# Kernel tuning notes

Hardware: AMD Instinct MI355X
Metric: run time of the kernel (lower is better)

## Reference

```python
import jax, jax.numpy as jnp
import numpy as np

B, L, D = 4, 2048, 64
N_HEAD = 4
LOCALITY = 0.2
PI = 3.141592653589793


def setup_inputs() -> dict:
    key = jax.random.key(0)
    k1, k2, k3 = jax.random.split(key, 3)
    mesh = jax.random.uniform(k1, (B, L, 2), dtype=jnp.float32)
    inputs = jax.random.normal(k2, (B, L, D), dtype=jnp.float32)
    lmda = jax.random.uniform(k3, (N_HEAD, 1, 1), dtype=jnp.float32)
    return {"mesh": mesh, "inputs": inputs, "lmda": lmda}


def reference(mesh, inputs, lmda):
    FMAX = jnp.finfo(jnp.float32).max
    # pairwise squared distances: (B, L, L)
    diff = mesh[:, :, None, :] - mesh[:, None, :, :]
    m_dist = jnp.sum(diff * diff, axis=-1)
    # per-head scale in (0, inf): tan(pi/4 * (1-eps) * (1 + sin(lmda)))
    scale = jnp.tan(0.25 * PI * (1.0 - 1e-07) * (1.0 + jnp.sin(lmda)))  # (H,1,1)
    scaled = m_dist[:, None, :, :] * scale  # (B, H, L, L)
    # row-wise quantile threshold (linear interpolation, matching torch.quantile)
    thresh = jnp.quantile(scaled, LOCALITY, axis=-1, keepdims=True)  # (B,H,L,1)
    masked = jnp.where(scaled <= thresh, scaled, FMAX)
    att = jax.nn.softmax(-masked, axis=-1)  # (B, H, L, L)
    # aggregate: (B,H,L,L) x (B,L,D) -> (B,L,H,D) -> (B,L,H*D)
    conv = jnp.einsum('bhnj,bjd->bnhd', att, inputs)
    conv = conv.reshape(inputs.shape[0], -1, N_HEAD * inputs.shape[-1])
    return jnp.concatenate([inputs, conv], axis=-1)
```

## Files before the change

kernel.cpp:

```cpp
#include <hip/hip_runtime.h>
#include <math.h>

#ifndef M_PI
#define M_PI 3.14159265358979323846
#endif

namespace {
constexpr int B_ = 4;
constexpr int L_ = 2048;
constexpr int D_ = 64;
constexpr int H_ = 4;
constexpr int RB = 8;
constexpr int KT = 64;
constexpr int NTILE = L_ / KT;
constexpr int CAPC = 256;
constexpr int OUTW = D_ + H_ * D_;
constexpr int APS = 2064;
}

typedef __attribute__((ext_vector_type(8))) short bf16x8;
typedef __attribute__((ext_vector_type(4))) float f32x4;

__device__ __forceinline__ unsigned bf16_rne(float x) {
    unsigned u = __float_as_uint(x);
    return (u + 0x7fffu + ((u >> 16) & 1u)) >> 16;
}

#define LDS_FENCE() __builtin_amdgcn_s_waitcnt(0xC07F)

__global__ __launch_bounds__(512, 8) void posatt_kernel(
    const float* __restrict__ mesh,
    const float* __restrict__ inputs,
    const float* __restrict__ lmda,
    float* __restrict__ out)
{
    __shared__ __align__(16) float2 s_mesh[L_];
    __shared__ __align__(16) char s_u1[16448];
    __shared__ float s_scale[H_];
    __shared__ float s_th[RB][H_];
    __shared__ float s_d409[RB], s_d410[RB];
    __shared__ float s_wsum[RB][H_];
    __shared__ unsigned s_ccw[8];

    const int t = threadIdx.x;
    const int l = t & 63;
    const int w = t >> 6;
    const int blk = blockIdx.x;
    const int b = blk >> 8;
    const int n0 = (blk & 255) * RB;

    if (t < H_) {
        const double lam = (double)lmda[t];
        const float C = (float)(0.25 * M_PI * (1.0 - 1e-07));
        const float s1 = (float)sin(lam);
        const float arg = __fmul_rn(C, __fadd_rn(1.0f, s1));
        s_scale[t] = (float)tan((double)arg);
    }
    {
        const float4* mg = reinterpret_cast<const float4*>(mesh + (size_t)b * L_ * 2);
        float4* msd = reinterpret_cast<float4*>(s_mesh);
        msd[t] = mg[t];
        msd[t + 512] = mg[t + 512];
    }
    __syncthreads();

    {
        unsigned* hw = reinterpret_cast<unsigned*>(s_u1) + w * 256;
        float* cw = reinterpret_cast<float*>(s_u1 + 8192) + w * CAPC;
        const int rl = w;
        const float2 me = s_mesh[n0 + rl];
        *reinterpret_cast<uint4*>(&hw[l * 4]) = make_uint4(0u, 0u, 0u, 0u);
        if (l == 0) s_ccw[w] = 0u;
        LDS_FENCE();
        #pragma unroll 1
        for (int it = 0; it < 32; ++it) {
            const int j = (it << 6) + l;
            const float2 mj = s_mesh[j];
            const float dx = __fsub_rn(me.x, mj.x);
            const float dy = __fsub_rn(me.y, mj.y);
            const float d = __fadd_rn(__fmul_rn(dx, dx), __fmul_rn(dy, dy));
            int bin = (int)(d * 128.0f); bin = bin < 255 ? bin : 255;
            atomicAdd(&hw[bin], 1u);
        }
        LDS_FENCE();
        const uint4 hv = *reinterpret_cast<const uint4*>(&hw[l * 4]);
        const unsigned p0 = hv.x, p1 = p0 + hv.y, p2 = p1 + hv.z, p3 = p2 + hv.w;
        unsigned sc = p3;
        #pragma unroll
        for (int off = 1; off < 64; off <<= 1) {
            const unsigned uu = __shfl_up(sc, off);
            if (l >= off) sc += uu;
        }
        const unsigned eb = sc - p3;
        const unsigned cum[4] = {eb + p0, eb + p1, eb + p2, eb + p3};
        int flo = -1, fhi = -1; unsigned fbase = 0u;
        #pragma unroll
        for (int e = 0; e < 4; ++e) {
            const unsigned prev = e ? cum[e - 1] : eb;
            if (cum[e] > 409u && prev <= 409u) { flo = l * 4 + e; fbase = prev; }
            if (cum[e] > 410u && prev <= 410u) { fhi = l * 4 + e; }
        }
        const unsigned long long bmlo = __ballot(flo >= 0);
        const int srclo = (int)__builtin_ctzll(bmlo);
        const int lo = __shfl(flo, srclo);
        const unsigned base = __shfl(fbase, srclo);
        const unsigned long long bmhi = __ballot(fhi >= 0);
        const int hi = __shfl(fhi, (int)__builtin_ctzll(bmhi));
        #pragma unroll 1
        for (int it = 0; it < 32; ++it) {
            const int j = (it << 6) + l;
            const float2 mj = s_mesh[j];
            const float dx = __fsub_rn(me.x, mj.x);
            const float dy = __fsub_rn(me.y, mj.y);
            const float d = __fadd_rn(__fmul_rn(dx, dx), __fmul_rn(dy, dy));
            int bin = (int)(d * 128.0f); bin = bin < 255 ? bin : 255;
            if (bin >= lo && bin <= hi) {
                const unsigned p = atomicAdd(&s_ccw[w], 1u);
                if (p < (unsigned)CAPC) cw[p] = d;
            }
        }
        LDS_FENCE();
        const int m = (int)min(s_ccw[w], (unsigned)CAPC);
        const int k409 = 409 - (int)base;
        const int k410 = 410 - (int)base;
        #pragma unroll 1
        for (int cc0 = 0; cc0 < m; cc0 += 64) {
            const int ci = cc0 + l;
            const float v = (ci < m) ? cw[ci] : 0.0f;
            int lt = 0, le = 0;
            #pragma unroll 1
            for (int i = 0; i < m; ++i) {
                const float u = cw[i];
                lt += (u < v) ? 1 : 0;
                le += (u <= v) ? 1 : 0;
            }
            if (ci < m) {
                if (lt <= k409 && k409 < le) s_d409[rl] = v;
                if (lt <= k410 && k410 < le) s_d410[rl] = v;
            }
        }
    }
    __syncthreads();

    if (t < RB * H_) {
        const int r = t >> 2, h = t & 3;
        const float scl = s_scale[h];
        const float s409 = __fmul_rn(s_d409[r], scl);
        const float s410 = __fmul_rn(s_d410[r], scl);
        const float pos = 0.2f * 2047.0f;
        const float g = pos - 409.0f;
        const float lw = 1.0f - g;
        s_th[r][h] = __fadd_rn(__fmul_rn(s409, lw), __fmul_rn(s410, g));
    }
    __syncthreads();

    const int mr   = t >> 4;
    const int h_b  = mr >> 3;
    const int r_b  = mr & 7;
    const int jg   = t & 15;
    const int row16 = ((h_b & 1) << 3) + r_b;
    const int pln   = h_b >> 1;
    const float2 me_b = s_mesh[n0 + r_b];
    const float sc_b = s_scale[h_b];
    const float th_b = s_th[r_b][h_b];
    const int aoff = pln * APS + ((((jg >> 3) * 4 + ((jg >> 1) & 3)) * 16 + row16) << 4) + ((jg & 1) << 3);
    float wacc = 0.0f;

    const int p_w  = w >> 2;
    const int ks_w = (w >> 1) & 1;
    const int nqh  = w & 1;
    f32x4 acc[2];
    acc[0] = (f32x4)0.0f; acc[1] = (f32x4)0.0f;

    const float* inpb = inputs + (size_t)b * L_ * D_;
    char* Abase = s_u1;
    char* Bbase = s_u1 + 2 * APS;

    #pragma unroll 1
    for (int tile = 0; tile < NTILE; ++tile) {
        __syncthreads();
        unsigned pk0[4];
        {
            const int kb0 = tile * KT + ((t >> 6) << 3);
            const float* pb0 = inpb + (size_t)kb0 * D_ + (t & 63);
            #pragma unroll
            for (int e2 = 0; e2 < 4; ++e2) {
                const float xa = pb0[(2 * e2) * D_];
                const float xb = pb0[(2 * e2 + 1) * D_];
                pk0[e2] = bf16_rne(xa) | (bf16_rne(xb) << 16);
            }
        }
        const int k0 = tile * KT;
        {
            const float4 mq0 = *reinterpret_cast<const float4*>(&s_mesh[k0 + jg * 4]);
            const float4 mq1 = *reinterpret_cast<const float4*>(&s_mesh[k0 + jg * 4 + 2]);
            const float dx0 = __fsub_rn(me_b.x, mq0.x);
            const float dy0 = __fsub_rn(me_b.y, mq0.y);
            const float d0 = __fadd_rn(__fmul_rn(dx0, dx0), __fmul_rn(dy0, dy0));
            const float dx1 = __fsub_rn(me_b.x, mq0.z);
            const float dy1 = __fsub_rn(me_b.y, mq0.w);
            const float d1 = __fadd_rn(__fmul_rn(dx1, dx1), __fmul_rn(dy1, dy1));
            const float dx2 = __fsub_rn(me_b.x, mq1.x);
            const float dy2 = __fsub_rn(me_b.y, mq1.y);
            const float d2 = __fadd_rn(__fmul_rn(dx2, dx2), __fmul_rn(dy2, dy2));
            const float dx3 = __fsub_rn(me_b.x, mq1.z);
            const float dy3 = __fsub_rn(me_b.y, mq1.w);
            const float d3 = __fadd_rn(__fmul_rn(dx3, dx3), __fmul_rn(dy3, dy3));
            const float x0 = __fmul_rn(d0, sc_b);
            const float x1 = __fmul_rn(d1, sc_b);
            const float x2 = __fmul_rn(d2, sc_b);
            const float x3 = __fmul_rn(d3, sc_b);
            const float w0 = (x0 <= th_b) ? __expf(-x0) : 0.0f;
            const float w1 = (x1 <= th_b) ? __expf(-x1) : 0.0f;
            const float w2 = (x2 <= th_b) ? __expf(-x2) : 0.0f;
            const float w3 = (x3 <= th_b) ? __expf(-x3) : 0.0f;
            wacc += (w0 + w1) + (w2 + w3);
            const unsigned u01 = bf16_rne(w0) | (bf16_rne(w1) << 16);
            const unsigned u23 = bf16_rne(w2) | (bf16_rne(w3) << 16);
            *reinterpret_cast<uint2*>(Abase + aoff) = make_uint2(u01, u23);
        }
        *reinterpret_cast<uint4*>(Bbase + t * 16) = make_uint4(pk0[0], pk0[1], pk0[2], pk0[3]);
        __syncthreads();
        const bf16x8 afr = *reinterpret_cast<const bf16x8*>(
            Abase + p_w * APS + (((ks_w * 4 + (l >> 4)) * 16 + (l & 15)) << 4));
        #pragma unroll
        for (int i = 0; i < 2; ++i) {
            const int nq = nqh * 2 + i;
            const bf16x8 bfr = *reinterpret_cast<const bf16x8*>(
                Bbase + (((ks_w * 4 + (l >> 4)) * 64 + nq * 16 + (l & 15)) << 4));
            acc[i] = __builtin_amdgcn_mfma_f32_16x16x32_bf16(afr, bfr, acc[i], 0, 0, 0);
        }
    }
    __syncthreads();

    wacc += __shfl_xor(wacc, 1);
    wacc += __shfl_xor(wacc, 2);
    wacc += __shfl_xor(wacc, 4);
    wacc += __shfl_xor(wacc, 8);
    if ((l & 15) == 0) s_wsum[r_b][h_b] = wacc;
    {
        float4* Cz = reinterpret_cast<float4*>(s_u1);
        Cz[t] = make_float4(0.f, 0.f, 0.f, 0.f);
    }
    __syncthreads();
    {
        float* Cf = reinterpret_cast<float*>(s_u1);
        #pragma unroll
        for (int i = 0; i < 2; ++i) {
            const int nq = nqh * 2 + i;
            #pragma unroll
            for (int reg = 0; reg < 4; ++reg) {
                const int row = (l >> 4) * 4 + reg;
                const int col = nq * 16 + (l & 15);
                atomicAdd(&Cf[(p_w * 16 + row) * 64 + col], acc[i][reg]);
            }
        }
    }
    __syncthreads();
    {
        const float* Cf = reinterpret_cast<const float*>(s_u1);
        const int pr = t >> 4;
        const int p = pr >> 4;
        const int row16o = pr & 15;
        const int h = p * 2 + (row16o >> 3);
        const int r = row16o & 7;
        const int col = (t & 15) << 2;
        const float wsv = s_wsum[r][h];
        const float inv = (wsv != 0.0f) ? 1.0f / wsv : 0.0f;
        float4 r0 = *reinterpret_cast<const float4*>(&Cf[pr * 64 + col]);
        r0.x *= inv; r0.y *= inv; r0.z *= inv; r0.w *= inv;
        float* op = out + (size_t)(b * L_ + n0 + r) * OUTW + D_ + h * 64 + col;
        *reinterpret_cast<float4*>(op) = r0;
    }
    {
        const int r = t >> 6;
        const int c = t & 63;
        out[(size_t)(b * L_ + n0 + r) * OUTW + c] = inpb[(size_t)(n0 + r) * D_ + c];
    }
}

extern "C" void kernel_launch(void* const* d_in, const int* in_sizes, int n_in,
                              void* d_out, int out_size, void* d_ws, size_t ws_size,
                              hipStream_t stream) {
    const float* mesh   = (const float*)d_in[0];
    const float* inputs = (const float*)d_in[1];
    const float* lmda   = (const float*)d_in[2];
    float* out = (float*)d_out;
    (void)in_sizes; (void)n_in; (void)out_size; (void)d_ws; (void)ws_size;
    hipLaunchKernelGGL(posatt_kernel, dim3(B_ * (L_ / RB)), dim3(512), 0, stream,
                       mesh, inputs, lmda, out);
}
```

Measured before the change: 146.5 us.

## Pre-convert inputs to bf16 tiled layout in a prep kernel; XOR-swizzle A tile in LDS

```diff
diff --git a/kernel.cpp b/kernel.cpp
--- a/kernel.cpp
+++ b/kernel.cpp
@@ -28,10 +28,37 @@
 
 #define LDS_FENCE() __builtin_amdgcn_s_waitcnt(0xC07F)
 
+__global__ __launch_bounds__(256) void prep_kernel(const float* __restrict__ inputs,
+                                                   char* __restrict__ ws) {
+    const int blk = blockIdx.x;
+    const int b = blk >> 6;
+    const int r6 = blk & 63;
+    const int tile = r6 >> 2;
+    const int qr = r6 & 3;
+    const int t = threadIdx.x;
+    const float* inb = inputs + ((size_t)b * L_ + tile * 128) * D_;
+    char* wsb = ws + (size_t)b * (L_ * D_ * 2) + tile * (128 * D_ * 2);
+    #pragma unroll
+    for (int i = 0; i < 4; ++i) {
+        const int idx = qr * 1024 + i * 256 + t;
+        const int n  = idx & 63;
+        const int kp = idx >> 6;
+        const int kl = kp << 1;
+        const float x0 = inb[kl * D_ + n];
+        const float x1 = inb[(kl + 1) * D_ + n];
+        const unsigned a = bf16_rne(x0);
+        const unsigned c = bf16_rne(x1);
+        const int chunk = (kl >> 3) * 64 + n;
+        const int e = kl & 7;
+        *reinterpret_cast<unsigned*>(wsb + chunk * 16 + e * 2) = a | (c << 16);
+    }
+}
+
 __global__ __launch_bounds__(512, 8) void posatt_kernel(
     const float* __restrict__ mesh,
     const float* __restrict__ inputs,
     const float* __restrict__ lmda,
+    const char* __restrict__ ws,
     float* __restrict__ out)
 {
     __shared__ __align__(16) float2 s_mesh[L_];
@@ -163,33 +190,30 @@
     const float2 me_b = s_mesh[n0 + r_b];
     const float sc_b = s_scale[h_b];
     const float th_b = s_th[r_b][h_b];
-    const int aoff = pln * APS + ((((jg >> 3) * 4 + ((jg >> 1) & 3)) * 16 + row16) << 4) + ((jg & 1) << 3);
+    const int ks4q_w = jg >> 1;
+    const int chunk_w = ks4q_w * 16 + row16;
+    const int chunkSw_w = chunk_w ^ (ks4q_w & 7);
+    const int aoff = pln * APS + (chunkSw_w << 4) + ((jg & 1) << 3);
     float wacc = 0.0f;
 
     const int p_w  = w >> 2;
     const int ks_w = (w >> 1) & 1;
     const int nqh  = w & 1;
+    const int ks4q_r = ks_w * 4 + (l >> 4);
+    const int chunk_r = ks4q_r * 16 + (l & 15);
+    const int aroff = p_w * APS + ((chunk_r ^ (ks4q_r & 7)) << 4);
     f32x4 acc[2];
     acc[0] = (f32x4)0.0f; acc[1] = (f32x4)0.0f;
 
     const float* inpb = inputs + (size_t)b * L_ * D_;
+    const char* wsb = ws + (size_t)b * (L_ * D_ * 2);
     char* Abase = s_u1;
     char* Bbase = s_u1 + 2 * APS;
 
     #pragma unroll 1
     for (int tile = 0; tile < NTILE; ++tile) {
         __syncthreads();
-        unsigned pk0[4];
-        {
-            const int kb0 = tile * KT + ((t >> 6) << 3);
-            const float* pb0 = inpb + (size_t)kb0 * D_ + (t & 63);
-            #pragma unroll
-            for (int e2 = 0; e2 < 4; ++e2) {
-                const float xa = pb0[(2 * e2) * D_];
-                const float xb = pb0[(2 * e2 + 1) * D_];
-                pk0[e2] = bf16_rne(xa) | (bf16_rne(xb) << 16);
-            }
-        }
+        const uint4 bg = *reinterpret_cast<const uint4*>(wsb + ((size_t)(tile * 512 + t) << 4));
         const int k0 = tile * KT;
         {
             const float4 mq0 = *reinterpret_cast<const float4*>(&s_mesh[k0 + jg * 4]);
@@ -219,10 +243,9 @@
             const unsigned u23 = bf16_rne(w2) | (bf16_rne(w3) << 16);
             *reinterpret_cast<uint2*>(Abase + aoff) = make_uint2(u01, u23);
         }
-        *reinterpret_cast<uint4*>(Bbase + t * 16) = make_uint4(pk0[0], pk0[1], pk0[2], pk0[3]);
+        *reinterpret_cast<uint4*>(Bbase + t * 16) = bg;
         __syncthreads();
-        const bf16x8 afr = *reinterpret_cast<const bf16x8*>(
-            Abase + p_w * APS + (((ks_w * 4 + (l >> 4)) * 16 + (l & 15)) << 4));
+        const bf16x8 afr = *reinterpret_cast<const bf16x8*>(Abase + aroff);
         #pragma unroll
         for (int i = 0; i < 2; ++i) {
             const int nq = nqh * 2 + i;
@@ -286,7 +309,9 @@
     const float* inputs = (const float*)d_in[1];
     const float* lmda   = (const float*)d_in[2];
     float* out = (float*)d_out;
-    (void)in_sizes; (void)n_in; (void)out_size; (void)d_ws; (void)ws_size;
+    char* ws = (char*)d_ws;
+    (void)in_sizes; (void)n_in; (void)out_size; (void)ws_size;
+    hipLaunchKernelGGL(prep_kernel, dim3(256), dim3(256), 0, stream, inputs, ws);
     hipLaunchKernelGGL(posatt_kernel, dim3(B_ * (L_ / RB)), dim3(512), 0, stream,
-                       mesh, inputs, lmda, out);
-}
+                       mesh, inputs, lmda, ws, out);
+}
```

Result: faster. 136.2 us (-7.0%).
